# Optimization experiments

Measured on AMD Instinct MI355X. Metric: run time of the kernel, lower is better.

## Reference

```python
import jax, jax.numpy as jnp
import numpy as np
from jax import lax

T, H, W = 2048, 128, 160


def setup_inputs() -> dict:
    key = jax.random.key(0)
    k1, = jax.random.split(key, 1)
    batch_x = jax.random.uniform(k1, (T, 1, H, W), dtype=jnp.float32)
    # params = [close, open, dhot] / 255 (defaults 1, 5, 8)
    params = jnp.array([1.0, 5.0, 8.0], dtype=jnp.float32) / 255.0
    HT0 = jnp.zeros((H, W), dtype=jnp.float32)
    LT0 = jnp.zeros((H, W), dtype=jnp.float32)
    # ConvTranspose2d(1,1,3,padding=1) with constant weight ones/(3**2/2) = 2/9;
    # symmetric kernel + padding=1 transposed conv == SAME-padded standard conv.
    kernel = jnp.full((1, 1, 3, 3), 2.0 / 9.0, dtype=jnp.float32)
    return {"batch_x": batch_x, "params": params, "HT0": HT0, "LT0": LT0, "kernel": kernel}


def reference(batch_x, params, HT0, LT0, kernel):
    d_close, d_open, d_hot = params[0], params[1], params[2]

    def step(carry, x):
        HT, LT = carry
        img = x[0]  # (H, W)
        # hot scores computed against *pre-update* thresholds
        tmpH_hot = jax.nn.sigmoid((img - HT - d_hot) * 500.0)
        tmpH = (img - HT) > 0
        HT = jnp.where(tmpH, HT + d_open, HT - d_close)
        tmpL_hot = jax.nn.sigmoid((LT - img - d_hot) * 500.0)
        tmpL = (LT - img) > 0
        LT = jnp.where(tmpL, LT - d_open, LT + d_close)
        return (HT, LT), tmpH_hot + tmpL_hot

    _, hot = lax.scan(step, (HT0, LT0), batch_x)  # hot: (T, H, W)

    # DiffErosion: relu(1 - conv(1 - x)) with SAME padding, batched over frames
    where_zero = (1.0 - hot)[:, None, :, :]  # (T, 1, H, W)
    sub = lax.conv_general_dilated(
        where_zero, kernel, window_strides=(1, 1), padding="SAME",
        dimension_numbers=("NCHW", "OIHW", "NCHW"))
    return jax.nn.relu(1.0 - sub)  # (T, 1, H, W)
```

## Files before the change

### kernel.cpp

```cpp
#include <hip/hip_runtime.h>


#define TILE_W 16
#define TILE_H 16
#define IN_W 14
#define IN_H 14
#define BUF 8
#define PRE 32

constexpr int T_FRAMES = 2048;
constexpr int H_IMG = 128;
constexpr int W_IMG = 160;
constexpr int HW = H_IMG * W_IMG;
constexpr float C1 = 721.3475204444817f;

constexpr size_t ws_needed(int snap) {
    return (size_t)(T_FRAMES / snap - 1) * HW * sizeof(float2);
}

__device__ __forceinline__ float dpp_from_left(float v) {
    return __int_as_float(__builtin_amdgcn_update_dpp(0, __float_as_int(v), 0x111, 0xF, 0xF, true));
}
__device__ __forceinline__ float dpp_from_right(float v) {
    return __int_as_float(__builtin_amdgcn_update_dpp(0, __float_as_int(v), 0x101, 0xF, 0xF, true));
}

#define S_ISSUE(V, F)                              \
    _Pragma("unroll")                              \
    for (int i = 0; i < PRE; ++i) V[i] = xp[((F) + i) * HW];

#define S_COMP(V)                                  \
    _Pragma("unroll")                              \
    for (int i = 0; i < PRE; ++i) {                \
        const float img = V[i];                    \
        HT = ((img - HT) > 0.0f) ? (HT + dO) : (HT - dC); \
        LT = ((LT - img) > 0.0f) ? (LT - dO) : (LT + dC); \
    }

template <int SNAP_>
__global__ __launch_bounds__(256, 1)
void svs_scan(const float* __restrict__ x, const float* __restrict__ params,
              const float* __restrict__ HT0, const float* __restrict__ LT0,
              float2* __restrict__ snap)
{
    constexpr int TEFF = T_FRAMES - SNAP_;
    const int pix = (int)blockIdx.x * 256 + (int)threadIdx.x;
    const float dC = params[0];
    const float dO = params[1];

    float HT = HT0[pix];
    float LT = LT0[pix];
    const float* xp = x + pix;

    auto maybe_snap = [&](int endf) {
        if ((endf % SNAP_) == 0) {
            const int k = endf / SNAP_ - 1;
            if (k < T_FRAMES / SNAP_ - 1)
                snap[(size_t)k * HW + pix] = make_float2(HT, LT);
        }
    };

    float va[PRE], vb[PRE], vc[PRE];
    S_ISSUE(va, 0)
    S_ISSUE(vb, PRE)
    __builtin_amdgcn_sched_barrier(0);

    for (int t = 0; t < TEFF; t += 3 * PRE) {
        if (t + 2 * PRE < TEFF) { S_ISSUE(vc, t + 2 * PRE) }
        __builtin_amdgcn_sched_barrier(0);
        S_COMP(va)
        maybe_snap(t + PRE);
        if (t + 3 * PRE < TEFF) { S_ISSUE(va, t + 3 * PRE) }
        __builtin_amdgcn_sched_barrier(0);
        if (t + PRE < TEFF) {
            S_COMP(vb)
            maybe_snap(t + 2 * PRE);
        }
        if (t + 4 * PRE < TEFF) { S_ISSUE(vb, t + 4 * PRE) }
        __builtin_amdgcn_sched_barrier(0);
        if (t + 2 * PRE < TEFF) {
            S_COMP(vc)
            maybe_snap(t + 3 * PRE);
        }
    }
}

template <int SNAP_>
__global__ __launch_bounds__(256)
void svs_compute(const float* __restrict__ x, const float* __restrict__ params,
                 const float* __restrict__ HT0, const float* __restrict__ LT0,
                 const float* __restrict__ kern, const float2* __restrict__ snap,
                 float* __restrict__ out)
{
    constexpr int NSLICE_ = T_FRAMES / SNAP_;
    constexpr int TOTAL_ = 120 * NSLICE_;
    const int lin = (int)blockIdx.x + 12 * (int)blockIdx.y + 120 * (int)blockIdx.z;
    const int w   = (lin & 7) * (TOTAL_ / 8) + (lin >> 3);
    const int bx  = w % 12;
    const int by  = (w / 12) % 10;
    const int slice = w / 120;

    const int tx = threadIdx.x & 15;
    const int ty = threadIdx.x >> 4;
    const int gx = bx * IN_W + tx - 1;
    const int gy = by * IN_H + ty - 1;
    const int t0 = slice * SNAP_;

    const bool valid = (gx >= 0) & (gx < W_IMG) & (gy >= 0) & (gy < H_IMG);
    const int cx = min(max(gx, 0), W_IMG - 1);
    const int cy = min(max(gy, 0), H_IMG - 1);
    const int pix = cy * W_IMG + cx;

    const float dC   = params[0];
    const float dO   = params[1];
    const float dHot = params[2];
    const float kw   = kern[4];
    const float c0   = dHot * C1;

    float HT, LT;
    if (slice == 0) {
        HT = valid ? HT0[pix] : 0.0f;
        LT = valid ? LT0[pix] : 0.0f;
    } else {
        const float2 s = snap[(size_t)(slice - 1) * HW + pix];
        HT = valid ? s.x : 0.0f;
        LT = valid ? s.y : 0.0f;
    }

    __shared__ float sm[TILE_H][BUF][TILE_W + 1];

    const bool doOut = (tx >= 1) & (tx <= IN_W) & (ty >= 1) & (ty <= IN_H) & valid;
    const int ym = max(ty - 1, 0);
    const int yp = min(ty + 1, TILE_H - 1);
    const float* xp = x + pix;
    float* op = out + pix;

    for (int tb = t0; tb < t0 + SNAP_; tb += BUF) {
        float v[BUF], hot[BUF];
        #pragma unroll
        for (int i = 0; i < BUF; ++i) v[i] = xp[(tb + i) * HW];
        #pragma unroll
        for (int i = 0; i < BUF; ++i) {
            const float img = v[i];
            const float aH = img - HT;
            const float eH = __builtin_amdgcn_exp2f(fmaf(aH, -C1, c0));
            const float hH = __builtin_amdgcn_rcpf(1.0f + eH);
            HT = (aH > 0.0f) ? (HT + dO) : (HT - dC);
            const float aL = LT - img;
            const float eL = __builtin_amdgcn_exp2f(fmaf(aL, -C1, c0));
            const float hL = __builtin_amdgcn_rcpf(1.0f + eL);
            LT = (aL > 0.0f) ? (LT - dO) : (LT + dC);
            hot[i] = valid ? (hH + hL) : 1.0f;
            sm[ty][i][tx] = hot[i];
        }
        __syncthreads();
        #pragma unroll
        for (int i = 0; i < BUF; ++i) {
            const float r0 = sm[ym][i][tx];
            const float r1 = sm[yp][i][tx];
            const float vs = r0 + hot[i] + r1;
            const float S  = vs + dpp_from_left(vs) + dpp_from_right(vs);
            float o = fmaf(S, kw, -1.0f);
            o = fmaxf(o, 0.0f);
            if (doOut) op[(tb + i) * HW] = o;
        }
        __syncthreads();
    }
}

extern "C" void kernel_launch(void* const* d_in, const int* in_sizes, int n_in,
                              void* d_out, int out_size, void* d_ws, size_t ws_size,
                              hipStream_t stream) {
    const float* x      = (const float*)d_in[0];
    const float* params = (const float*)d_in[1];
    const float* HT0p   = (const float*)d_in[2];
    const float* LT0p   = (const float*)d_in[3];
    const float* kern   = (const float*)d_in[4];
    float* out = (float*)d_out;

    if (ws_size >= ws_needed(64)) {
        float2* snap = (float2*)d_ws;
        svs_scan<64><<<dim3(HW / 256), dim3(256), 0, stream>>>(x, params, HT0p, LT0p, snap);
        svs_compute<64><<<dim3(12, 10, T_FRAMES / 64), dim3(256), 0, stream>>>(
            x, params, HT0p, LT0p, kern, snap, out);
    } else if (ws_size >= ws_needed(128)) {
        float2* snap = (float2*)d_ws;
        svs_scan<128><<<dim3(HW / 256), dim3(256), 0, stream>>>(x, params, HT0p, LT0p, snap);
        svs_compute<128><<<dim3(12, 10, T_FRAMES / 128), dim3(256), 0, stream>>>(
            x, params, HT0p, LT0p, kern, snap, out);
    } else {
        svs_compute<2048><<<dim3(12, 10, 1), dim3(256), 0, stream>>>(
            x, params, HT0p, LT0p, kern, (const float2*)d_ws, out);
    }
}
```

Measured before the change: 145.0 us.

## Split scan into single-wave blocks processing two pixels per thread

Adds a new scan kernel for the default snapshot interval. Each thread loads float2 pairs and advances two independent HT/LT recurrences, giving it more instruction-level parallelism. It launches 160 single-wavefront blocks instead of 80 blocks of 256 threads, so the serial threshold scan is spread over more compute units. Snapshots are written as float4 in a layout that matches the float2 indexing the compute kernel already uses. The compute kernel's frame buffer per barrier also grows from 8 to 16, which halves its syncs but raises register pressure.

```diff
diff --git a/kernel.cpp b/kernel.cpp
--- a/kernel.cpp
+++ b/kernel.cpp
@@ -5,13 +5,15 @@
 #define TILE_H 16
 #define IN_W 14
 #define IN_H 14
-#define BUF 8
-#define PRE 32
+#define BUF 16
+#define PRE2 16
 
 constexpr int T_FRAMES = 2048;
 constexpr int H_IMG = 128;
 constexpr int W_IMG = 160;
 constexpr int HW = H_IMG * W_IMG;
+constexpr int SNAP = 64;
+constexpr int TEFF = T_FRAMES - SNAP;
 constexpr float C1 = 721.3475204444817f;
 
 constexpr size_t ws_needed(int snap) {
@@ -25,62 +27,54 @@
     return __int_as_float(__builtin_amdgcn_update_dpp(0, __float_as_int(v), 0x101, 0xF, 0xF, true));
 }
 
-#define S_ISSUE(V, F)                              \
-    _Pragma("unroll")                              \
-    for (int i = 0; i < PRE; ++i) V[i] = xp[((F) + i) * HW];
-
-#define S_COMP(V)                                  \
-    _Pragma("unroll")                              \
-    for (int i = 0; i < PRE; ++i) {                \
-        const float img = V[i];                    \
-        HT = ((img - HT) > 0.0f) ? (HT + dO) : (HT - dC); \
-        LT = ((LT - img) > 0.0f) ? (LT - dO) : (LT + dC); \
-    }
-
-template <int SNAP_>
-__global__ __launch_bounds__(256, 1)
-void svs_scan(const float* __restrict__ x, const float* __restrict__ params,
-              const float* __restrict__ HT0, const float* __restrict__ LT0,
-              float2* __restrict__ snap)
+__global__ __launch_bounds__(64, 1)
+void svs_scan2(const float* __restrict__ x, const float* __restrict__ params,
+               const float* __restrict__ HT0, const float* __restrict__ LT0,
+               float4* __restrict__ snap4)
 {
-    constexpr int TEFF = T_FRAMES - SNAP_;
-    const int pix = (int)blockIdx.x * 256 + (int)threadIdx.x;
+    const int pix2 = (int)blockIdx.x * 64 + (int)threadIdx.x;
     const float dC = params[0];
     const float dO = params[1];
 
-    float HT = HT0[pix];
-    float LT = LT0[pix];
-    const float* xp = x + pix;
-
-    auto maybe_snap = [&](int endf) {
-        if ((endf % SNAP_) == 0) {
-            const int k = endf / SNAP_ - 1;
-            if (k < T_FRAMES / SNAP_ - 1)
-                snap[(size_t)k * HW + pix] = make_float2(HT, LT);
-        }
-    };
-
-    float va[PRE], vb[PRE], vc[PRE];
-    S_ISSUE(va, 0)
-    S_ISSUE(vb, PRE)
+    const float2 h0 = ((const float2*)HT0)[pix2];
+    const float2 l0 = ((const float2*)LT0)[pix2];
+    float HTx = h0.x, HTy = h0.y, LTx = l0.x, LTy = l0.y;
+    const float2* xp2 = (const float2*)x + pix2;
+
+    float2 va[PRE2], vb[PRE2];
+    #pragma unroll
+    for (int i = 0; i < PRE2; ++i) va[i] = xp2[i * (HW / 2)];
     __builtin_amdgcn_sched_barrier(0);
 
-    for (int t = 0; t < TEFF; t += 3 * PRE) {
-        if (t + 2 * PRE < TEFF) { S_ISSUE(vc, t + 2 * PRE) }
-        __builtin_amdgcn_sched_barrier(0);
-        S_COMP(va)
-        maybe_snap(t + PRE);
-        if (t + 3 * PRE < TEFF) { S_ISSUE(va, t + 3 * PRE) }
-        __builtin_amdgcn_sched_barrier(0);
-        if (t + PRE < TEFF) {
-            S_COMP(vb)
-            maybe_snap(t + 2 * PRE);
-        }
-        if (t + 4 * PRE < TEFF) { S_ISSUE(vb, t + 4 * PRE) }
-        __builtin_amdgcn_sched_barrier(0);
-        if (t + 2 * PRE < TEFF) {
-            S_COMP(vc)
-            maybe_snap(t + 3 * PRE);
+    for (int t = 0; t < TEFF; t += 2 * PRE2) {
+        #pragma unroll
+        for (int i = 0; i < PRE2; ++i) vb[i] = xp2[(t + PRE2 + i) * (HW / 2)];
+        __builtin_amdgcn_sched_barrier(0);
+        #pragma unroll
+        for (int i = 0; i < PRE2; ++i) {
+            const float ix = va[i].x, iy = va[i].y;
+            HTx = ((ix - HTx) > 0.0f) ? (HTx + dO) : (HTx - dC);
+            LTx = ((LTx - ix) > 0.0f) ? (LTx - dO) : (LTx + dC);
+            HTy = ((iy - HTy) > 0.0f) ? (HTy + dO) : (HTy - dC);
+            LTy = ((LTy - iy) > 0.0f) ? (LTy - dO) : (LTy + dC);
+        }
+        if (t + 2 * PRE2 < TEFF) {
+            #pragma unroll
+            for (int i = 0; i < PRE2; ++i) va[i] = xp2[(t + 2 * PRE2 + i) * (HW / 2)];
+        }
+        __builtin_amdgcn_sched_barrier(0);
+        #pragma unroll
+        for (int i = 0; i < PRE2; ++i) {
+            const float ix = vb[i].x, iy = vb[i].y;
+            HTx = ((ix - HTx) > 0.0f) ? (HTx + dO) : (HTx - dC);
+            LTx = ((LTx - ix) > 0.0f) ? (LTx - dO) : (LTx + dC);
+            HTy = ((iy - HTy) > 0.0f) ? (HTy + dO) : (HTy - dC);
+            LTy = ((LTy - iy) > 0.0f) ? (LTy - dO) : (LTy + dC);
+        }
+        if (((t + 2 * PRE2) & (SNAP - 1)) == 0) {
+            const int k = (t + 2 * PRE2) / SNAP - 1;
+            if (k < T_FRAMES / SNAP - 1)
+                snap4[(size_t)k * (HW / 2) + pix2] = make_float4(HTx, LTx, HTy, LTy);
         }
     }
 }
@@ -92,8 +86,7 @@
                  const float* __restrict__ kern, const float2* __restrict__ snap,
                  float* __restrict__ out)
 {
-    constexpr int NSLICE_ = T_FRAMES / SNAP_;
-    constexpr int TOTAL_ = 120 * NSLICE_;
+    constexpr int TOTAL_ = 120 * (T_FRAMES / SNAP_);
     const int lin = (int)blockIdx.x + 12 * (int)blockIdx.y + 120 * (int)blockIdx.z;
     const int w   = (lin & 7) * (TOTAL_ / 8) + (lin >> 3);
     const int bx  = w % 12;
@@ -168,6 +161,61 @@
     }
 }
 
+template <int SNAP_>
+__global__ __launch_bounds__(256, 1)
+void svs_scan(const float* __restrict__ x, const float* __restrict__ params,
+              const float* __restrict__ HT0, const float* __restrict__ LT0,
+              float2* __restrict__ snap)
+{
+    constexpr int PRE = 32;
+    constexpr int TEFF_ = T_FRAMES - SNAP_;
+    const int pix = (int)blockIdx.x * 256 + (int)threadIdx.x;
+    const float dC = params[0];
+    const float dO = params[1];
+
+    float HT = HT0[pix];
+    float LT = LT0[pix];
+    const float* xp = x + pix;
+
+    float va[PRE], vb[PRE];
+    #pragma unroll
+    for (int i = 0; i < PRE; ++i) va[i] = xp[i * HW];
+    __builtin_amdgcn_sched_barrier(0);
+
+    for (int t = 0; t < TEFF_; t += 2 * PRE) {
+        #pragma unroll
+        for (int i = 0; i < PRE; ++i) vb[i] = xp[(t + PRE + i) * HW];
+        __builtin_amdgcn_sched_barrier(0);
+        #pragma unroll
+        for (int i = 0; i < PRE; ++i) {
+            const float img = va[i];
+            HT = ((img - HT) > 0.0f) ? (HT + dO) : (HT - dC);
+            LT = ((LT - img) > 0.0f) ? (LT - dO) : (LT + dC);
+        }
+        if (((t + PRE) % SNAP_) == 0) {
+            const int k = (t + PRE) / SNAP_ - 1;
+            if (k >= 0 && k < T_FRAMES / SNAP_ - 1)
+                snap[(size_t)k * HW + pix] = make_float2(HT, LT);
+        }
+        if (t + 2 * PRE < TEFF_) {
+            #pragma unroll
+            for (int i = 0; i < PRE; ++i) va[i] = xp[(t + 2 * PRE + i) * HW];
+        }
+        __builtin_amdgcn_sched_barrier(0);
+        #pragma unroll
+        for (int i = 0; i < PRE; ++i) {
+            const float img = vb[i];
+            HT = ((img - HT) > 0.0f) ? (HT + dO) : (HT - dC);
+            LT = ((LT - img) > 0.0f) ? (LT - dO) : (LT + dC);
+        }
+        if (((t + 2 * PRE) % SNAP_) == 0) {
+            const int k = (t + 2 * PRE) / SNAP_ - 1;
+            if (k < T_FRAMES / SNAP_ - 1)
+                snap[(size_t)k * HW + pix] = make_float2(HT, LT);
+        }
+    }
+}
+
 extern "C" void kernel_launch(void* const* d_in, const int* in_sizes, int n_in,
                               void* d_out, int out_size, void* d_ws, size_t ws_size,
                               hipStream_t stream) {
@@ -179,10 +227,10 @@
     float* out = (float*)d_out;
 
     if (ws_size >= ws_needed(64)) {
-        float2* snap = (float2*)d_ws;
-        svs_scan<64><<<dim3(HW / 256), dim3(256), 0, stream>>>(x, params, HT0p, LT0p, snap);
+        svs_scan2<<<dim3(HW / 128), dim3(64), 0, stream>>>(
+            x, params, HT0p, LT0p, (float4*)d_ws);
         svs_compute<64><<<dim3(12, 10, T_FRAMES / 64), dim3(256), 0, stream>>>(
-            x, params, HT0p, LT0p, kern, snap, out);
+            x, params, HT0p, LT0p, kern, (const float2*)d_ws, out);
     } else if (ws_size >= ws_needed(128)) {
         float2* snap = (float2*)d_ws;
         svs_scan<128><<<dim3(HW / 256), dim3(256), 0, stream>>>(x, params, HT0p, LT0p, snap);
```

Result: slower. 187.3 us (+29.2%).
